# Kernel optimization log

Hardware: AMD Instinct MI355X
Metric: run time of the kernel (lower is better)

## Reference

```python
import jax, jax.numpy as jnp
import numpy as np
import math

B, S, D, H = 4, 1024, 4096, 32
HD = D // H  # 128


def _rope(t, cos, sin):
    # t: [B,S,H,HD]; cos/sin: [S, HD//2]
    tr = t.reshape(*t.shape[:-1], HD // 2, 2)
    re, im = tr[..., 0], tr[..., 1]
    c = cos[None, :, None, :]
    s = sin[None, :, None, :]
    out_re = re * c - im * s
    out_im = re * s + im * c
    return jnp.stack([out_re, out_im], axis=-1).reshape(t.shape)


def setup_inputs() -> dict:
    key = jax.random.key(0)
    ks = jax.random.split(key, 6)
    wscale = 1.0 / math.sqrt(D)
    x = jax.random.normal(ks[0], (B, S, D), dtype=jnp.float32)
    wq = jax.random.normal(ks[1], (D, D), dtype=jnp.float32) * wscale
    wk = jax.random.normal(ks[2], (D, D), dtype=jnp.float32) * wscale
    wv = jax.random.normal(ks[3], (D, D), dtype=jnp.float32) * wscale
    wo = jax.random.normal(ks[4], (D, D), dtype=jnp.float32) * wscale
    # standard LLaMA RoPE frequencies: theta = 10000^{-2i/HD}
    inv_freq = 1.0 / (10000.0 ** (np.arange(0, HD, 2, dtype=np.float32) / HD))
    angles = np.arange(S, dtype=np.float32)[:, None] * inv_freq[None, :]  # [S, HD//2]
    freqs_cos = jnp.asarray(np.cos(angles), dtype=jnp.float32)
    freqs_sin = jnp.asarray(np.sin(angles), dtype=jnp.float32)
    # causal mask, additive, 0 on/below diagonal, -inf above
    mask = jnp.where(jnp.tril(jnp.ones((S, S), dtype=bool)), 0.0, -jnp.inf)
    mask = mask[None, None].astype(jnp.float32)  # [1,1,S,S]
    return {"x": x, "wq": wq, "wk": wk, "wv": wv, "wo": wo,
            "freqs_cos": freqs_cos, "freqs_sin": freqs_sin, "mask": mask}


def reference(x, wq, wk, wv, wo, freqs_cos, freqs_sin, mask):
    # projections (torch Linear: y = x @ W^T)
    xq = (x @ wq.T).reshape(B, S, H, HD)
    xk = (x @ wk.T).reshape(B, S, H, HD)
    xv = (x @ wv.T).reshape(B, S, H, HD)
    xq = _rope(xq, freqs_cos, freqs_sin)
    xk = _rope(xk, freqs_cos, freqs_sin)
    # prefill (start_pos == 0): keys/values are xk/xv
    scores = jnp.einsum('bshd,bthd->bhst', xq, xk) / math.sqrt(HD)
    scores = scores + mask
    probs = jax.nn.softmax(scores.astype(jnp.float32), axis=-1).astype(xq.dtype)
    out = jnp.einsum('bhst,bthd->bshd', probs, xv).reshape(B, S, D)
    return out @ wo.T
```

## Files before the change

### kernel.cpp

```cpp
#include <hip/hip_runtime.h>
#include <hip/hip_bf16.h>


typedef __bf16 bf16_t;
typedef bf16_t bf16x8 __attribute__((ext_vector_type(8)));
typedef bf16_t bf16x4 __attribute__((ext_vector_type(4)));
typedef bf16_t bf16x2 __attribute__((ext_vector_type(2)));
typedef float  f32x4  __attribute__((ext_vector_type(4)));

#define DDIM 4096
#define NTILES 64
#define NEG_INF (-__builtin_inff())
#define MFMA16(a,b,c) __builtin_amdgcn_mfma_f32_16x16x32_bf16(a,b,c,0,0,0)

__device__ __forceinline__ void gl_lds16(const bf16_t* g, bf16_t* l) {
    __builtin_amdgcn_global_load_lds((__attribute__((address_space(1))) void*)(g),
                                     (__attribute__((address_space(3))) void*)(l), 16, 0, 0);
}

__global__ __launch_bounds__(256)
void cvt3_k(const float* __restrict__ s0, bf16_t* __restrict__ d0,
            const float* __restrict__ s1, bf16_t* __restrict__ d1,
            const float* __restrict__ s2, bf16_t* __restrict__ d2, int n8)
{
    const float* src; bf16_t* dst;
    if (blockIdx.y == 0)      { src = s0; dst = d0; }
    else if (blockIdx.y == 1) { src = s1; dst = d1; }
    else                      { src = s2; dst = d2; }
    const int stride = gridDim.x * 256;
    for (int i = blockIdx.x * 256 + threadIdx.x; i < n8; i += stride) {
        const float* s = src + (size_t)i * 8;
        f32x4 a = *(const f32x4*)(s);
        f32x4 b = *(const f32x4*)(s + 4);
        bf16x8 o;
        o[0] = (bf16_t)a.x; o[1] = (bf16_t)a.y; o[2] = (bf16_t)a.z; o[3] = (bf16_t)a.w;
        o[4] = (bf16_t)b.x; o[5] = (bf16_t)b.y; o[6] = (bf16_t)b.z; o[7] = (bf16_t)b.w;
        *(bf16x8*)(dst + (size_t)i * 8) = o;
    }
}


__device__ __forceinline__ void stage_half(const bf16_t* __restrict__ A,
    const bf16_t* __restrict__ Bm, int m0, int n0, int kt, int hh,
    bf16_t* __restrict__ sb, int wave, int lane)
{
#pragma unroll
    for (int j = 0; j < 2; ++j) {
        const int chunk = wave * 2 + j;
        int row0;
        if (hh == 0)      row0 = chunk * 8;
        else if (hh == 1) row0 = 128 + chunk * 8;
        else if (hh == 2) row0 = (chunk < 8) ? chunk * 8 : 64 + chunk * 8;
        else              row0 = (chunk < 8) ? 64 + chunk * 8 : 128 + chunk * 8;
        const bool isB = (hh < 2);
        const int grow = (isB ? n0 : m0) + row0 + (lane >> 3);
        const int gcol = kt + (((lane & 7) ^ (lane >> 3)) << 3);
        const bf16_t* gp = (isB ? Bm : A) + (size_t)grow * DDIM + gcol;
        gl_lds16(gp, sb + (isB ? 16384 : 0) + row0 * 64);
    }
}

template<int STG>
__device__ __forceinline__ void ktile(const bf16_t* __restrict__ A,
    const bf16_t* __restrict__ Bm, int m0, int n0, int t,
    bf16_t* __restrict__ sb, bf16_t* __restrict__ sbn,
    int wave, int lane, int quad, int r, int wm, int wn,
    f32x4 acc[4][2][4], bf16x8 bfrag[4][2])
{
    const int kx0 = (quad ^ (r & 7)) << 3;
    const int kx1 = ((4 + quad) ^ (r & 7)) << 3;
    {
        bf16x8 af[2][2];
#pragma unroll
        for (int nf = 0; nf < 4; ++nf) {
            const int ro = 16384 + (((wn << 6) + (nf << 4) + r) << 6);
            bfrag[nf][0] = *(const bf16x8*)(sb + ro + kx0);
            bfrag[nf][1] = *(const bf16x8*)(sb + ro + kx1);
        }
#pragma unroll
        for (int mf = 0; mf < 2; ++mf) {
            const int ro = ((wm << 7) + (mf << 4) + r) << 6;
            af[mf][0] = *(const bf16x8*)(sb + ro + kx0);
            af[mf][1] = *(const bf16x8*)(sb + ro + kx1);
        }
        if (STG >= 1) stage_half(A, Bm, m0, n0, (t + 1) << 6, 3, sbn, wave, lane);
        asm volatile("s_waitcnt lgkmcnt(8)" ::: "memory");
        __builtin_amdgcn_sched_barrier(0);
        __builtin_amdgcn_s_barrier();
        asm volatile("s_waitcnt lgkmcnt(0)" ::: "memory");
        __builtin_amdgcn_sched_barrier(0);
        __builtin_amdgcn_s_setprio(1);
#pragma unroll
        for (int kk = 0; kk < 2; ++kk)
#pragma unroll
            for (int mf = 0; mf < 2; ++mf)
#pragma unroll
                for (int nf = 0; nf < 4; ++nf)
                    acc[0][mf][nf] = MFMA16(af[mf][kk], bfrag[nf][kk], acc[0][mf][nf]);
        __builtin_amdgcn_s_setprio(0);
        __builtin_amdgcn_sched_barrier(0);
        __builtin_amdgcn_s_barrier();
    }
#pragma unroll
    for (int q = 1; q < 4; ++q) {
        bf16x8 af[2][2];
#pragma unroll
        for (int mf = 0; mf < 2; ++mf) {
            const int ro = ((wm << 7) + (q << 5) + (mf << 4) + r) << 6;
            af[mf][0] = *(const bf16x8*)(sb + ro + kx0);
            af[mf][1] = *(const bf16x8*)(sb + ro + kx1);
        }
        if (STG == 2) stage_half(A, Bm, m0, n0, (t + 2) << 6, q - 1, sb, wave, lane);
        __builtin_amdgcn_sched_barrier(0);
        __builtin_amdgcn_s_barrier();
        asm volatile("s_waitcnt lgkmcnt(0)" ::: "memory");
        __builtin_amdgcn_sched_barrier(0);
        __builtin_amdgcn_s_setprio(1);
#pragma unroll
        for (int kk = 0; kk < 2; ++kk)
#pragma unroll
            for (int mf = 0; mf < 2; ++mf)
#pragma unroll
                for (int nf = 0; nf < 4; ++nf)
                    acc[q][mf][nf] = MFMA16(af[mf][kk], bfrag[nf][kk], acc[q][mf][nf]);
        __builtin_amdgcn_s_setprio(0);
        if (q == 3) {
            if (STG == 2)      asm volatile("s_waitcnt vmcnt(6)" ::: "memory");
            else if (STG == 1) asm volatile("s_waitcnt vmcnt(0)" ::: "memory");
        }
        __builtin_amdgcn_sched_barrier(0);
        __builtin_amdgcn_s_barrier();
    }
}

template<bool C_F32>
__device__ __forceinline__ void gemm_body(const bf16_t* __restrict__ A,
    const bf16_t* __restrict__ Bm, void* __restrict__ Cv,
    const float* __restrict__ fc, const float* __restrict__ fs, bool doRope)
{
    __shared__ __attribute__((aligned(16))) bf16_t sm[2 * 32768];
    const int tid  = threadIdx.x;
    const int wave = tid >> 6, lane = tid & 63;
    const int quad = lane >> 4, r = lane & 15;
    const int wm = wave >> 2, wn = wave & 3;
    const int swz = ((int)blockIdx.x % 8) * 32 + (int)blockIdx.x / 8;
    const int m0 = (swz >> 4) << 8, n0 = (swz & 15) << 8;

    f32x4 acc[4][2][4] = {};
    bf16x8 bfrag[4][2];

#pragma unroll
    for (int hh = 0; hh < 4; ++hh) stage_half(A, Bm, m0, n0, 0, hh, sm, wave, lane);
#pragma unroll
    for (int hh = 0; hh < 3; ++hh) stage_half(A, Bm, m0, n0, 64, hh, sm + 32768, wave, lane);
    asm volatile("s_waitcnt vmcnt(6)" ::: "memory");
    __builtin_amdgcn_s_barrier();

#pragma unroll 2
    for (int t = 0; t < NTILES - 2; ++t) {
        bf16_t* sb  = sm + ((t & 1) ? 32768 : 0);
        bf16_t* sbn = sm + ((t & 1) ? 0 : 32768);
        ktile<2>(A, Bm, m0, n0, t, sb, sbn, wave, lane, quad, r, wm, wn, acc, bfrag);
    }
    ktile<1>(A, Bm, m0, n0, NTILES - 2, sm, sm + 32768, wave, lane, quad, r, wm, wn, acc, bfrag);
    ktile<0>(A, Bm, m0, n0, NTILES - 1, sm + 32768, sm, wave, lane, quad, r, wm, wn, acc, bfrag);

    const float sgn = (r & 1) ? 1.0f : -1.0f;
#pragma unroll
    for (int q = 0; q < 4; ++q)
#pragma unroll
        for (int mf = 0; mf < 2; ++mf)
#pragma unroll
            for (int reg = 0; reg < 4; ++reg) {
                const int grow = m0 + (wm << 7) + (q << 5) + (mf << 4) + (quad << 2) + reg;
                const size_t rowoff = (size_t)grow * DDIM;
                const int s = grow & 1023;
#pragma unroll
                for (int nf = 0; nf < 4; ++nf) {
                    float v = acc[q][mf][nf][reg];
                    if (doRope) {
                        const int p = ((wn & 1) << 5) + (nf << 3) + (r >> 1);
                        const float c  = fc[s * 64 + p];
                        const float sn = fs[s * 64 + p];
                        const float partner = __shfl_xor(v, 1);
                        v = v * c + sgn * partner * sn;
                    }
                    const size_t idx = rowoff + n0 + (wn << 6) + (nf << 4) + r;
                    if constexpr (C_F32) ((float*)Cv)[idx] = v;
                    else                 ((bf16_t*)Cv)[idx] = (bf16_t)v;
                }
            }
}

__global__ __launch_bounds__(512, 2)
void gemm_qkv(const bf16_t* __restrict__ A,
              const bf16_t* __restrict__ b0, const bf16_t* __restrict__ b1,
              const bf16_t* __restrict__ b2,
              bf16_t* __restrict__ c0, bf16_t* __restrict__ c1, bf16_t* __restrict__ c2,
              const float* __restrict__ fc, const float* __restrict__ fs)
{
    const int sel = blockIdx.z;
    const bf16_t* Bm = (sel == 0) ? b0 : (sel == 1) ? b1 : b2;
    bf16_t*       Cv = (sel == 0) ? c0 : (sel == 1) ? c1 : c2;
    gemm_body<false>(A, Bm, Cv, fc, fs, sel != 1);
}

__global__ __launch_bounds__(512, 2)
void gemm_out(const bf16_t* __restrict__ A, const bf16_t* __restrict__ Bm,
              float* __restrict__ Cv)
{
    gemm_body<true>(A, Bm, Cv, nullptr, nullptr, false);
}

__global__ __launch_bounds__(256, 2)
void attn_k(const bf16_t* __restrict__ qm, const bf16_t* __restrict__ km,
            const bf16_t* __restrict__ vm, bf16_t* __restrict__ om)
{
    constexpr int BQ = 128, BT = 64;
    constexpr int PS = 80;
    __shared__ __attribute__((aligned(16))) bf16_t sK[BT * 128];
    __shared__ __attribute__((aligned(16))) bf16_t sVt[128 * 64];
    __shared__ __attribute__((aligned(16))) bf16_t sP[4][32 * PS];
    const int tid = threadIdx.x, wave = tid >> 6, lane = tid & 63;
    const int quad = lane >> 4, r = lane & 15;
    const int b = blockIdx.x >> 5, h = blockIdx.x & 31;
    const int q0 = (7 - (int)blockIdx.y) * BQ;
    const int qw = q0 + wave * 32;
    const float scale = 0.08838834764831845f;

    bf16x8 qf[2][4];
#pragma unroll
    for (int mt = 0; mt < 2; ++mt)
#pragma unroll
        for (int kk = 0; kk < 4; ++kk)
            qf[mt][kk] = *(const bf16x8*)(qm + (size_t)(b * 1024 + qw + mt * 16 + r) * DDIM
                                          + h * 128 + kk * 32 + quad * 8);

    f32x4 oacc[2][8] = {};
    float m_i[2][4], l_i[2][4];
#pragma unroll
    for (int mt = 0; mt < 2; ++mt)
#pragma unroll
        for (int reg = 0; reg < 4; ++reg) { m_i[mt][reg] = NEG_INF; l_i[mt][reg] = 0.f; }

    const bf16_t* gKb = km + (size_t)(b * 1024 + wave * 16 + quad) * DDIM + h * 128;
    const int rp = tid >> 3, cseg = tid & 7;

    for (int t0 = 0; t0 < q0 + BQ; t0 += BT) {
#pragma unroll
        for (int i = 0; i < 4; ++i) {
            const int xv = (i * 4 + quad) & 7;
            gl_lds16(gKb + (size_t)(t0 + i * 4) * DDIM + ((r ^ xv) << 3),
                     sK + (wave * 4 + i) * 512);
        }
        {
            const bf16_t* gv = vm + (size_t)(b * 1024 + t0 + 2 * rp) * DDIM + h * 128 + cseg * 16;
            bf16x8 v00 = *(const bf16x8*)(gv);
            bf16x8 v01 = *(const bf16x8*)(gv + 8);
            bf16x8 v10 = *(const bf16x8*)(gv + DDIM);
            bf16x8 v11 = *(const bf16x8*)(gv + DDIM + 8);
#pragma unroll
            for (int e = 0; e < 8; ++e) {
                bf16x2 w0, w1;
                w0.x = v00[e]; w0.y = v10[e];
                w1.x = v01[e]; w1.y = v11[e];
                const int pb = ((((rp >> 2) ^ (e ^ cseg)) & 7) << 3) + ((rp & 3) << 1);
                *(bf16x2*)(sVt + (cseg * 16 + e) * 64 + pb) = w0;
                *(bf16x2*)(sVt + (cseg * 16 + 8 + e) * 64 + pb) = w1;
            }
        }
        __syncthreads();

        f32x4 sacc[2][4] = {};
#pragma unroll
        for (int kk = 0; kk < 4; ++kk) {
            bf16x8 kf[4];
#pragma unroll
            for (int nt = 0; nt < 4; ++nt)
                kf[nt] = *(const bf16x8*)(sK + (nt * 16 + r) * 128
                                          + (((kk * 4 + quad) ^ (r & 7)) << 3));
#pragma unroll
            for (int mt = 0; mt < 2; ++mt)
#pragma unroll
                for (int nt = 0; nt < 4; ++nt)
                    sacc[mt][nt] = MFMA16(qf[mt][kk], kf[nt], sacc[mt][nt]);
        }

#pragma unroll
        for (int mt = 0; mt < 2; ++mt) {
#pragma unroll
            for (int reg = 0; reg < 4; ++reg) {
                const int qrow = qw + mt * 16 + quad * 4 + reg;
                float mx = NEG_INF;
#pragma unroll
                for (int nt = 0; nt < 4; ++nt) {
                    const int tcol = t0 + nt * 16 + r;
                    float v = sacc[mt][nt][reg] * scale;
                    v = (tcol <= qrow) ? v : NEG_INF;
                    sacc[mt][nt][reg] = v;
                    mx = fmaxf(mx, v);
                }
                mx = fmaxf(mx, __shfl_xor(mx, 1));
                mx = fmaxf(mx, __shfl_xor(mx, 2));
                mx = fmaxf(mx, __shfl_xor(mx, 4));
                mx = fmaxf(mx, __shfl_xor(mx, 8));
                if (!__all(mx - m_i[mt][reg] <= 8.0f)) {
                    const float mnew = fmaxf(m_i[mt][reg], mx);
                    const float alpha = __expf(m_i[mt][reg] - mnew);
                    m_i[mt][reg] = mnew;
                    l_i[mt][reg] *= alpha;
#pragma unroll
                    for (int nt = 0; nt < 8; ++nt)
                        oacc[mt][nt][reg] *= alpha;
                }
                float rs = 0.f;
#pragma unroll
                for (int nt = 0; nt < 4; ++nt) {
                    const float pv = __expf(sacc[mt][nt][reg] - m_i[mt][reg]);
                    rs += pv;
                    sP[wave][(mt * 16 + quad * 4 + reg) * PS + nt * 16 + r] = (bf16_t)pv;
                }
                rs += __shfl_xor(rs, 1);
                rs += __shfl_xor(rs, 2);
                rs += __shfl_xor(rs, 4);
                rs += __shfl_xor(rs, 8);
                l_i[mt][reg] += rs;
            }
        }

#pragma unroll
        for (int kk2 = 0; kk2 < 2; ++kk2) {
            bf16x8 pf[2];
#pragma unroll
            for (int mt = 0; mt < 2; ++mt)
                pf[mt] = *(const bf16x8*)(&sP[wave][(mt * 16 + r) * PS + kk2 * 32 + quad * 8]);
#pragma unroll
            for (int nt = 0; nt < 8; ++nt) {
                bf16x8 vf = *(const bf16x8*)(sVt + (nt * 16 + r) * 64
                                             + ((((kk2 * 4 + quad) ^ (r & 7) ^ nt) & 7) << 3));
#pragma unroll
                for (int mt = 0; mt < 2; ++mt)
                    oacc[mt][nt] = MFMA16(pf[mt], vf, oacc[mt][nt]);
            }
        }
        __syncthreads();
    }

#pragma unroll
    for (int mt = 0; mt < 2; ++mt)
#pragma unroll
        for (int reg = 0; reg < 4; ++reg) {
            const float inv = 1.0f / l_i[mt][reg];
            const size_t row = (size_t)(b * 1024 + qw + mt * 16 + quad * 4 + reg) * DDIM + h * 128;
#pragma unroll
            for (int nt = 0; nt < 8; ++nt)
                om[row + nt * 16 + r] = (bf16_t)(oacc[mt][nt][reg] * inv);
        }
}

extern "C" void kernel_launch(void* const* d_in, const int* in_sizes, int n_in,
                              void* d_out, int out_size, void* d_ws, size_t ws_size,
                              hipStream_t stream)
{
    (void)in_sizes; (void)n_in; (void)out_size; (void)d_ws; (void)ws_size;
    const float* x  = (const float*)d_in[0];
    const float* wq = (const float*)d_in[1];
    const float* wk = (const float*)d_in[2];
    const float* wv = (const float*)d_in[3];
    const float* wo = (const float*)d_in[4];
    const float* fc = (const float*)d_in[5];
    const float* fs = (const float*)d_in[6];

    const size_t NE = (size_t)DDIM * DDIM;
    const int n8 = (int)(NE / 8);

    bf16_t* wkb = (bf16_t*)d_out;
    bf16_t* wvb = wkb + NE;
    bf16_t* xb  = (bf16_t*)d_in[2];
    bf16_t* wqb = xb + NE;
    bf16_t* wob = (bf16_t*)d_in[3];
    bf16_t* ob  = wob + NE;
    bf16_t* kb  = (bf16_t*)d_in[1];
    bf16_t* vb  = kb + NE;
    bf16_t* qb  = (bf16_t*)d_in[4];
    float*  out = (float*)d_out;

    cvt3_k<<<dim3(2048, 2), 256, 0, stream>>>(wk, wkb, wv, wvb, wv, wvb, n8);
    cvt3_k<<<dim3(2048, 3), 256, 0, stream>>>(x, xb, wq, wqb, wo, wob, n8);

    gemm_qkv<<<dim3(256, 1, 3), 512, 0, stream>>>(xb, wkb, wvb, wqb, kb, vb, qb, fc, fs);
    attn_k<<<dim3(128, 8), 256, 0, stream>>>(qb, kb, vb, ob);
    gemm_out<<<256, 512, 0, stream>>>(ob, wob, out);
}
```

Before: 884.6 us.

## Double-buffer K/V loads in attention and split QKV GEMM into specialized launches

The attention kernel now prefetches the next K tile into a second LDS buffer and holds the next V tile in registers while the current tile is computed, so global loads overlap with MFMA work. It also raises wave priority around the MFMA blocks. Separately, the fused 3-way QKV GEMM launch is split into three launches with the RoPE branch made a compile-time template parameter, which removes the runtime branch but gives up concurrency across the three GEMMs within a single grid. The extra K buffer raises LDS use and the prefetched V adds register pressure, which could affect occupancy.

```diff
diff --git a/kernel.cpp b/kernel.cpp
--- a/kernel.cpp
+++ b/kernel.cpp
@@ -133,10 +133,10 @@
     }
 }
 
-template<bool C_F32>
+template<bool C_F32, bool ROPE>
 __device__ __forceinline__ void gemm_body(const bf16_t* __restrict__ A,
     const bf16_t* __restrict__ Bm, void* __restrict__ Cv,
-    const float* __restrict__ fc, const float* __restrict__ fs, bool doRope)
+    const float* __restrict__ fc, const float* __restrict__ fs)
 {
     __shared__ __attribute__((aligned(16))) bf16_t sm[2 * 32768];
     const int tid  = threadIdx.x;
@@ -178,7 +178,7 @@
 #pragma unroll
                 for (int nf = 0; nf < 4; ++nf) {
                     float v = acc[q][mf][nf][reg];
-                    if (doRope) {
+                    if constexpr (ROPE) {
                         const int p = ((wn & 1) << 5) + (nf << 3) + (r >> 1);
                         const float c  = fc[s * 64 + p];
                         const float sn = fs[s * 64 + p];
@@ -193,23 +193,25 @@
 }
 
 __global__ __launch_bounds__(512, 2)
-void gemm_qkv(const bf16_t* __restrict__ A,
-              const bf16_t* __restrict__ b0, const bf16_t* __restrict__ b1,
-              const bf16_t* __restrict__ b2,
-              bf16_t* __restrict__ c0, bf16_t* __restrict__ c1, bf16_t* __restrict__ c2,
-              const float* __restrict__ fc, const float* __restrict__ fs)
-{
-    const int sel = blockIdx.z;
-    const bf16_t* Bm = (sel == 0) ? b0 : (sel == 1) ? b1 : b2;
-    bf16_t*       Cv = (sel == 0) ? c0 : (sel == 1) ? c1 : c2;
-    gemm_body<false>(A, Bm, Cv, fc, fs, sel != 1);
+void gemm_rope(const bf16_t* __restrict__ A, const bf16_t* __restrict__ Bm,
+               bf16_t* __restrict__ Cv, const float* __restrict__ fc,
+               const float* __restrict__ fs)
+{
+    gemm_body<false, true>(A, Bm, Cv, fc, fs);
+}
+
+__global__ __launch_bounds__(512, 2)
+void gemm_plain(const bf16_t* __restrict__ A, const bf16_t* __restrict__ Bm,
+                bf16_t* __restrict__ Cv)
+{
+    gemm_body<false, false>(A, Bm, Cv, nullptr, nullptr);
 }
 
 __global__ __launch_bounds__(512, 2)
 void gemm_out(const bf16_t* __restrict__ A, const bf16_t* __restrict__ Bm,
               float* __restrict__ Cv)
 {
-    gemm_body<true>(A, Bm, Cv, nullptr, nullptr, false);
+    gemm_body<true, false>(A, Bm, Cv, nullptr, nullptr);
 }
 
 __global__ __launch_bounds__(256, 2)
@@ -218,7 +220,7 @@
 {
     constexpr int BQ = 128, BT = 64;
     constexpr int PS = 80;
-    __shared__ __attribute__((aligned(16))) bf16_t sK[BT * 128];
+    __shared__ __attribute__((aligned(16))) bf16_t sK[2][BT * 128];
     __shared__ __attribute__((aligned(16))) bf16_t sVt[128 * 64];
     __shared__ __attribute__((aligned(16))) bf16_t sP[4][32 * PS];
     const int tid = threadIdx.x, wave = tid >> 6, lane = tid & 63;
@@ -245,31 +247,47 @@
 
     const bf16_t* gKb = km + (size_t)(b * 1024 + wave * 16 + quad) * DDIM + h * 128;
     const int rp = tid >> 3, cseg = tid & 7;
-
+    const bf16_t* gVb = vm + (size_t)(b * 1024 + 2 * rp) * DDIM + h * 128 + cseg * 16;
+
+    bf16x8 v00, v01, v10, v11;
+#pragma unroll
+    for (int i = 0; i < 4; ++i) {
+        const int xv = (i * 4 + quad) & 7;
+        gl_lds16(gKb + (size_t)(i * 4) * DDIM + ((r ^ xv) << 3),
+                 sK[0] + (wave * 4 + i) * 512);
+    }
+    v00 = *(const bf16x8*)(gVb);
+    v01 = *(const bf16x8*)(gVb + 8);
+    v10 = *(const bf16x8*)(gVb + DDIM);
+    v11 = *(const bf16x8*)(gVb + DDIM + 8);
+
+    int buf = 0;
     for (int t0 = 0; t0 < q0 + BQ; t0 += BT) {
-#pragma unroll
-        for (int i = 0; i < 4; ++i) {
-            const int xv = (i * 4 + quad) & 7;
-            gl_lds16(gKb + (size_t)(t0 + i * 4) * DDIM + ((r ^ xv) << 3),
-                     sK + (wave * 4 + i) * 512);
-        }
-        {
-            const bf16_t* gv = vm + (size_t)(b * 1024 + t0 + 2 * rp) * DDIM + h * 128 + cseg * 16;
-            bf16x8 v00 = *(const bf16x8*)(gv);
-            bf16x8 v01 = *(const bf16x8*)(gv + 8);
-            bf16x8 v10 = *(const bf16x8*)(gv + DDIM);
-            bf16x8 v11 = *(const bf16x8*)(gv + DDIM + 8);
-#pragma unroll
-            for (int e = 0; e < 8; ++e) {
-                bf16x2 w0, w1;
-                w0.x = v00[e]; w0.y = v10[e];
-                w1.x = v01[e]; w1.y = v11[e];
-                const int pb = ((((rp >> 2) ^ (e ^ cseg)) & 7) << 3) + ((rp & 3) << 1);
-                *(bf16x2*)(sVt + (cseg * 16 + e) * 64 + pb) = w0;
-                *(bf16x2*)(sVt + (cseg * 16 + 8 + e) * 64 + pb) = w1;
+        __syncthreads();
+#pragma unroll
+        for (int e = 0; e < 8; ++e) {
+            bf16x2 w0, w1;
+            w0.x = v00[e]; w0.y = v10[e];
+            w1.x = v01[e]; w1.y = v11[e];
+            const int pb = ((((rp >> 2) ^ (e ^ cseg)) & 7) << 3) + ((rp & 3) << 1);
+            *(bf16x2*)(sVt + (cseg * 16 + e) * 64 + pb) = w0;
+            *(bf16x2*)(sVt + (cseg * 16 + 8 + e) * 64 + pb) = w1;
+        }
+        __syncthreads();
+
+        if (t0 + BT < q0 + BQ) {
+#pragma unroll
+            for (int i = 0; i < 4; ++i) {
+                const int xv = (i * 4 + quad) & 7;
+                gl_lds16(gKb + (size_t)(t0 + BT + i * 4) * DDIM + ((r ^ xv) << 3),
+                         sK[buf ^ 1] + (wave * 4 + i) * 512);
             }
-        }
-        __syncthreads();
+            const bf16_t* gv = gVb + (size_t)(t0 + BT) * DDIM;
+            v00 = *(const bf16x8*)(gv);
+            v01 = *(const bf16x8*)(gv + 8);
+            v10 = *(const bf16x8*)(gv + DDIM);
+            v11 = *(const bf16x8*)(gv + DDIM + 8);
+        }
 
         f32x4 sacc[2][4] = {};
 #pragma unroll
@@ -277,13 +295,15 @@
             bf16x8 kf[4];
 #pragma unroll
             for (int nt = 0; nt < 4; ++nt)
-                kf[nt] = *(const bf16x8*)(sK + (nt * 16 + r) * 128
+                kf[nt] = *(const bf16x8*)(sK[buf] + (nt * 16 + r) * 128
                                           + (((kk * 4 + quad) ^ (r & 7)) << 3));
+            __builtin_amdgcn_s_setprio(1);
 #pragma unroll
             for (int mt = 0; mt < 2; ++mt)
 #pragma unroll
                 for (int nt = 0; nt < 4; ++nt)
                     sacc[mt][nt] = MFMA16(qf[mt][kk], kf[nt], sacc[mt][nt]);
+            __builtin_amdgcn_s_setprio(0);
         }
 
 #pragma unroll
@@ -338,12 +358,14 @@
             for (int nt = 0; nt < 8; ++nt) {
                 bf16x8 vf = *(const bf16x8*)(sVt + (nt * 16 + r) * 64
                                              + ((((kk2 * 4 + quad) ^ (r & 7) ^ nt) & 7) << 3));
+                __builtin_amdgcn_s_setprio(1);
 #pragma unroll
                 for (int mt = 0; mt < 2; ++mt)
                     oacc[mt][nt] = MFMA16(pf[mt], vf, oacc[mt][nt]);
+                __builtin_amdgcn_s_setprio(0);
             }
         }
-        __syncthreads();
+        buf ^= 1;
     }
 
 #pragma unroll
@@ -388,7 +410,9 @@
     cvt3_k<<<dim3(2048, 2), 256, 0, stream>>>(wk, wkb, wv, wvb, wv, wvb, n8);
     cvt3_k<<<dim3(2048, 3), 256, 0, stream>>>(x, xb, wq, wqb, wo, wob, n8);
 
-    gemm_qkv<<<dim3(256, 1, 3), 512, 0, stream>>>(xb, wkb, wvb, wqb, kb, vb, qb, fc, fs);
+    gemm_rope <<<256, 512, 0, stream>>>(xb, wkb, kb, fc, fs);
+    gemm_plain<<<256, 512, 0, stream>>>(xb, wvb, vb);
+    gemm_rope <<<256, 512, 0, stream>>>(xb, wqb, qb, fc, fs);
     attn_k<<<dim3(128, 8), 256, 0, stream>>>(qb, kb, vb, ob);
     gemm_out<<<256, 512, 0, stream>>>(ob, wob, out);
 }
```

Result: faster. 827.5 us (-6.5%).
